# Performance work log

Measured on AMD Instinct MI355X. Metric: run time of the kernel, lower is better.

The kernel has to match this reference:

```python
import jax, jax.numpy as jnp
import numpy as np

PADDING_IDX = 0
SMOOTHING = 0.1


def setup_inputs() -> dict:
    key = jax.random.key(0)
    k1, k2 = jax.random.split(key)
    N, V = 4096, 32000
    # x plays the role of log-probabilities [N, V]
    x = jax.random.normal(k1, (N, V), dtype=jnp.float32)
    target = jax.random.randint(k2, (N,), 0, V, dtype=jnp.int64)
    return {"x": x, "target": target}


def reference(x, target):
    n = x.shape[-1]
    mask = (target != PADDING_IDX)  # [N] valid-token mask
    maskf = mask.astype(x.dtype)
    # smooth term: -sum over vocab of x, zeroed for padding rows, summed over batch
    loss = -jnp.sum(x * maskf[:, None])
    # nll term: gather log-prob at target class, ignore padding rows, sum
    gathered = jnp.take_along_axis(x, target[:, None], axis=1)[:, 0]  # [N]
    nll = -jnp.sum(gathered * maskf)
    return SMOOTHING * (loss / n) + (1.0 - SMOOTHING) * nll
```

## Files before the change

### kernel.cpp

```cpp
#include <hip/hip_runtime.h>


#define LS_V 32000
#define LS_V4 8000
#define LS_SMOOTH 0.1f

typedef float f4 __attribute__((ext_vector_type(4)));

__global__ __launch_bounds__(256) void ls_row_reduce(
    const float* __restrict__ x,
    const int*   __restrict__ target,
    float*       __restrict__ partial)
{
    const int row = blockIdx.x;
    const int tid = threadIdx.x;

    const int t = target[row];
    const float g = x[(size_t)row * LS_V + t];

    const f4* __restrict__ xr = (const f4*)(x + (size_t)row * LS_V);

    float s0 = 0.0f, s1 = 0.0f;
    int j = tid;
    #pragma unroll 5
    for (int i = 0; i < 15; ++i, j += 512) {
        f4 a = __builtin_nontemporal_load(&xr[j]);
        f4 b = __builtin_nontemporal_load(&xr[j + 256]);
        s0 += (a.x + a.y) + (a.z + a.w);
        s1 += (b.x + b.y) + (b.z + b.w);
    }
    {
        f4 a = __builtin_nontemporal_load(&xr[j]);
        s0 += (a.x + a.y) + (a.z + a.w);
        if (tid < 64) {
            f4 b = __builtin_nontemporal_load(&xr[j + 256]);
            s1 += (b.x + b.y) + (b.z + b.w);
        }
    }

    float s = s0 + s1;
    #pragma unroll
    for (int off = 32; off > 0; off >>= 1)
        s += __shfl_down(s, off, 64);

    __shared__ float wsum[4];
    if ((tid & 63) == 0) wsum[tid >> 6] = s;
    __syncthreads();

    if (tid == 0) {
        const float S = (wsum[0] + wsum[1]) + (wsum[2] + wsum[3]);
        const float maskf = (t != 0) ? 1.0f : 0.0f;
        partial[row] = maskf * (-(LS_SMOOTH / (float)LS_V) * S
                                - (1.0f - LS_SMOOTH) * g);
    }
}

__global__ __launch_bounds__(256) void ls_final(
    const float* __restrict__ partial,
    float*       __restrict__ out,
    int n)
{
    const int tid = threadIdx.x;
    float s = 0.0f;
    for (int i = tid; i < n; i += 256) s += partial[i];

    #pragma unroll
    for (int off = 32; off > 0; off >>= 1)
        s += __shfl_down(s, off, 64);

    __shared__ float wsum[4];
    if ((tid & 63) == 0) wsum[tid >> 6] = s;
    __syncthreads();
    if (tid == 0) out[0] = (wsum[0] + wsum[1]) + (wsum[2] + wsum[3]);
}

extern "C" void kernel_launch(void* const* d_in, const int* in_sizes, int n_in,
                              void* d_out, int out_size, void* d_ws, size_t ws_size,
                              hipStream_t stream)
{
    const float* x      = (const float*)d_in[0];
    const int*   target = (const int*)d_in[1];
    float*       out    = (float*)d_out;
    float*       part   = (float*)d_ws;

    const int N = in_sizes[1];

    ls_row_reduce<<<N, 256, 0, stream>>>(x, target, part);
    ls_final<<<1, 256, 0, stream>>>(part, out, N);
}
```

Before: 628.9 us.

## Replace per-row reduction with grid-stride flat sweep and chunked partial sums

```diff
diff --git a/kernel.cpp b/kernel.cpp
--- a/kernel.cpp
+++ b/kernel.cpp
@@ -1,68 +1,57 @@
 #include <hip/hip_runtime.h>
 
 
-#define LS_V 32000
-#define LS_V4 8000
+#define LS_V      32000
+#define LS_V4     8000
 #define LS_SMOOTH 0.1f
+
+#define SW_BLOCKS  2000
+#define SW_THREADS 256
+#define SW_TOTAL   (SW_BLOCKS * SW_THREADS)
 
 typedef float f4 __attribute__((ext_vector_type(4)));
 
-__global__ __launch_bounds__(256) void ls_row_reduce(
+__global__ __launch_bounds__(SW_THREADS) void ls_sweep(
     const float* __restrict__ x,
-    const int*   __restrict__ target,
-    float*       __restrict__ partial)
+    float*       __restrict__ chunksum,
+    int nf4)
 {
-    const int row = blockIdx.x;
-    const int tid = threadIdx.x;
+    const int g    = blockIdx.x * SW_THREADS + threadIdx.x;
+    const int lane = threadIdx.x & 63;
+    const f4* __restrict__ x4 = (const f4*)x;
 
-    const int t = target[row];
-    const float g = x[(size_t)row * LS_V + t];
-
-    const f4* __restrict__ xr = (const f4*)(x + (size_t)row * LS_V);
-
-    float s0 = 0.0f, s1 = 0.0f;
-    int j = tid;
-    #pragma unroll 5
-    for (int i = 0; i < 15; ++i, j += 512) {
-        f4 a = __builtin_nontemporal_load(&xr[j]);
-        f4 b = __builtin_nontemporal_load(&xr[j + 256]);
-        s0 += (a.x + a.y) + (a.z + a.w);
-        s1 += (b.x + b.y) + (b.z + b.w);
-    }
-    {
-        f4 a = __builtin_nontemporal_load(&xr[j]);
-        s0 += (a.x + a.y) + (a.z + a.w);
-        if (tid < 64) {
-            f4 b = __builtin_nontemporal_load(&xr[j + 256]);
-            s1 += (b.x + b.y) + (b.z + b.w);
-        }
-    }
-
-    float s = s0 + s1;
-    #pragma unroll
-    for (int off = 32; off > 0; off >>= 1)
-        s += __shfl_down(s, off, 64);
-
-    __shared__ float wsum[4];
-    if ((tid & 63) == 0) wsum[tid >> 6] = s;
-    __syncthreads();
-
-    if (tid == 0) {
-        const float S = (wsum[0] + wsum[1]) + (wsum[2] + wsum[3]);
-        const float maskf = (t != 0) ? 1.0f : 0.0f;
-        partial[row] = maskf * (-(LS_SMOOTH / (float)LS_V) * S
-                                - (1.0f - LS_SMOOTH) * g);
+    #pragma unroll 4
+    for (int f4idx = g; f4idx < nf4; f4idx += SW_TOTAL) {
+        f4 v = __builtin_nontemporal_load(&x4[f4idx]);
+        float s = (v.x + v.y) + (v.z + v.w);
+        #pragma unroll
+        for (int off = 32; off > 0; off >>= 1)
+            s += __shfl_down(s, off, 64);
+        if (lane == 0)
+            chunksum[f4idx >> 6] = s;
     }
 }
 
-__global__ __launch_bounds__(256) void ls_final(
-    const float* __restrict__ partial,
-    float*       __restrict__ out,
-    int n)
+__global__ __launch_bounds__(256) void ls_finish1(
+    const float* __restrict__ x,
+    const int*   __restrict__ target,
+    const float* __restrict__ chunksum,
+    float*       __restrict__ bsum)
 {
     const int tid = threadIdx.x;
-    float s = 0.0f;
-    for (int i = tid; i < n; i += 256) s += partial[i];
+    const int r   = blockIdx.x * 256 + tid;
+
+    const int   t = target[r];
+    const float g = x[(size_t)r * LS_V + t];
+
+    const float* __restrict__ cs = chunksum + r * (LS_V4 / 64);
+    float rs = 0.0f;
+    #pragma unroll 5
+    for (int i = 0; i < (LS_V4 / 64); ++i) rs += cs[i];
+
+    float s = (t != 0) ? (-(LS_SMOOTH / (float)LS_V) * rs
+                          - (1.0f - LS_SMOOTH) * g)
+                       : 0.0f;
 
     #pragma unroll
     for (int off = 32; off > 0; off >>= 1)
@@ -71,7 +60,21 @@
     __shared__ float wsum[4];
     if ((tid & 63) == 0) wsum[tid >> 6] = s;
     __syncthreads();
-    if (tid == 0) out[0] = (wsum[0] + wsum[1]) + (wsum[2] + wsum[3]);
+    if (tid == 0)
+        bsum[blockIdx.x] = (wsum[0] + wsum[1]) + (wsum[2] + wsum[3]);
+}
+
+__global__ __launch_bounds__(64) void ls_finish2(
+    const float* __restrict__ bsum,
+    float*       __restrict__ out,
+    int nb)
+{
+    const int tid = threadIdx.x;
+    float s = (tid < nb) ? bsum[tid] : 0.0f;
+    #pragma unroll
+    for (int off = 32; off > 0; off >>= 1)
+        s += __shfl_down(s, off, 64);
+    if (tid == 0) out[0] = s;
 }
 
 extern "C" void kernel_launch(void* const* d_in, const int* in_sizes, int n_in,
@@ -81,10 +84,16 @@
     const float* x      = (const float*)d_in[0];
     const int*   target = (const int*)d_in[1];
     float*       out    = (float*)d_out;
-    float*       part   = (float*)d_ws;
 
-    const int N = in_sizes[1];
+    const int N    = in_sizes[1];
+    const int nf4  = N * LS_V4;
+    const int nchk = nf4 >> 6;
+    const int nb   = N / 256;
 
-    ls_row_reduce<<<N, 256, 0, stream>>>(x, target, part);
-    ls_final<<<1, 256, 0, stream>>>(part, out, N);
+    float* chunksum = (float*)d_ws;
+    float* bsum     = chunksum + nchk;
+
+    ls_sweep  <<<SW_BLOCKS, SW_THREADS, 0, stream>>>(x, chunksum, nf4);
+    ls_finish1<<<nb,        256,        0, stream>>>(x, target, chunksum, bsum);
+    ls_finish2<<<1,         64,         0, stream>>>(bsum, out, nb);
 }
```

Measured after the change: 644.8 us. 2.5% more time.
